# Kernel optimization log

Measured on AMD Instinct MI355X. Metric: run time of the kernel, lower is better.

## Reference

```python
import jax, jax.numpy as jnp
import numpy as np

N_WEIGHTS = 16777216  # 2**24
BATCH = 16777216
PRIOR_SIGMA = 1.0
HALF_LOG_2PI = 0.9189385332046727  # 0.5 * log(2*pi)


def _normal_logprob(x, mu, sigma):
    # Gaussian log density, elementwise
    z = (x - mu) / sigma
    return -0.5 * z * z - jnp.log(sigma) - HALF_LOG_2PI


def setup_inputs() -> dict:
    key = jax.random.key(0)
    k1, k2, k3, k4, k5 = jax.random.split(key, 5)
    noisy_weights = jax.random.normal(k1, (N_WEIGHTS,), dtype=jnp.float32)
    mu_weights = jax.random.normal(k2, (N_WEIGHTS,), dtype=jnp.float32)
    # strictly positive sigmas in [0.5, 1.5)
    sigma_weights = jax.random.uniform(k3, (N_WEIGHTS,), dtype=jnp.float32) + 0.5
    mu_prediction = jax.random.normal(k4, (BATCH,), dtype=jnp.float32)
    sigma_prediction = jnp.float32(0.7)  # single scalar value
    y_true = jax.random.normal(k5, (BATCH,), dtype=jnp.float32)
    return {
        "noisy_weights": noisy_weights,
        "mu_weights": mu_weights,
        "sigma_weights": sigma_weights,
        "mu_prediction": mu_prediction,
        "sigma_prediction": sigma_prediction,
        "y_true": y_true,
    }


def reference(noisy_weights, mu_weights, sigma_weights, mu_prediction, sigma_prediction, y_true):
    # log p(w) under prior N(0, prior_sigma), summed
    loss_prior = _normal_logprob(noisy_weights, 0.0, jnp.float32(PRIOR_SIGMA)).sum()
    # log N(y_true | mu_prediction, sigma_prediction), summed over batch
    loss_likelihood = _normal_logprob(y_true, mu_prediction, sigma_prediction).sum()
    # log q(w | mu_weights, sigma_weights), summed over weights
    loss_variational = _normal_logprob(noisy_weights, mu_weights, sigma_weights).sum()
    # total = variational - prior - likelihood (negative ELBO)
    return loss_variational - loss_prior - loss_likelihood
```

## Files before the change

kernel.cpp:

```cpp
#include <hip/hip_runtime.h>


constexpr int THREADS = 256;
constexpr int ITERS   = 4;
constexpr float LN2          = 0.6931471805599453f;
constexpr float HALF_LOG_2PI = 0.9189385332046727f;

__global__ __launch_bounds__(THREADS, 4) void elbo_partial_fixed(
    const float* __restrict__ xw,
    const float* __restrict__ muw,
    const float* __restrict__ sgw,
    const float* __restrict__ mup,
    const float* __restrict__ sp_ptr,
    const float* __restrict__ yt,
    float* __restrict__ partial)
{
    const float4* x4 = (const float4*)xw;
    const float4* m4 = (const float4*)muw;
    const float4* s4 = (const float4*)sgw;
    const float4* p4 = (const float4*)mup;
    const float4* y4 = (const float4*)yt;

    const int base = blockIdx.x * (THREADS * ITERS) + threadIdx.x;

    float4 xv[ITERS], mv[ITERS], sv[ITERS], pv[ITERS], yv[ITERS];
#pragma unroll
    for (int it = 0; it < ITERS; ++it) {
        int i = base + it * THREADS;
        xv[it] = x4[i];
        mv[it] = m4[i];
        sv[it] = s4[i];
        pv[it] = p4[i];
        yv[it] = y4[i];
    }

    float aw = 0.f;
    float al = 0.f;
    float ab = 0.f;
#pragma unroll
    for (int it = 0; it < ITERS; ++it) {
#define COMP(c) {                                        \
        float dx = xv[it].c - mv[it].c;                  \
        float r  = __builtin_amdgcn_rcpf(sv[it].c);      \
        float z  = dx * r;                               \
        aw += xv[it].c * xv[it].c - z * z;               \
        al += __log2f(sv[it].c);                         \
        float d  = yv[it].c - pv[it].c;                  \
        ab += d * d; }
        COMP(x) COMP(y) COMP(z) COMP(w)
#undef COMP
    }

    float sp = sp_ptr[0];
    float inv2sp2 = 0.5f * __builtin_amdgcn_rcpf(sp * sp);
    float v = 0.5f * aw - LN2 * al + inv2sp2 * ab;

    for (int off = 32; off > 0; off >>= 1)
        v += __shfl_down(v, off);

    __shared__ float lds[THREADS / 64];
    int lane = threadIdx.x & 63;
    int wave = threadIdx.x >> 6;
    if (lane == 0) lds[wave] = v;
    __syncthreads();
    if (threadIdx.x == 0)
        partial[blockIdx.x] = lds[0] + lds[1] + lds[2] + lds[3];
}

__global__ __launch_bounds__(THREADS) void elbo_partial_generic(
    const float* __restrict__ xw,
    const float* __restrict__ muw,
    const float* __restrict__ sgw,
    const float* __restrict__ mup,
    const float* __restrict__ sp_ptr,
    const float* __restrict__ yt,
    float* __restrict__ partial,
    int n4)
{
    const float4* x4 = (const float4*)xw;
    const float4* m4 = (const float4*)muw;
    const float4* s4 = (const float4*)sgw;
    const float4* p4 = (const float4*)mup;
    const float4* y4 = (const float4*)yt;

    float aw = 0.f, al = 0.f, ab = 0.f;
    int idx    = blockIdx.x * blockDim.x + threadIdx.x;
    int stride = gridDim.x * blockDim.x;
    for (int i = idx; i < n4; i += stride) {
        float4 xv = x4[i], mv = m4[i], sv = s4[i], pv = p4[i], yv = y4[i];
#define COMP(c) {                                   \
        float dx = xv.c - mv.c;                     \
        float r  = __builtin_amdgcn_rcpf(sv.c);     \
        float z  = dx * r;                          \
        aw += xv.c * xv.c - z * z;                  \
        al += __log2f(sv.c);                        \
        float d  = yv.c - pv.c;                     \
        ab += d * d; }
        COMP(x) COMP(y) COMP(z) COMP(w)
#undef COMP
    }
    float sp = sp_ptr[0];
    float inv2sp2 = 0.5f * __builtin_amdgcn_rcpf(sp * sp);
    float v = 0.5f * aw - LN2 * al + inv2sp2 * ab;

    for (int off = 32; off > 0; off >>= 1)
        v += __shfl_down(v, off);

    __shared__ float lds[THREADS / 64];
    int lane = threadIdx.x & 63;
    int wave = threadIdx.x >> 6;
    if (lane == 0) lds[wave] = v;
    __syncthreads();
    if (threadIdx.x == 0)
        partial[blockIdx.x] = lds[0] + lds[1] + lds[2] + lds[3];
}

__global__ __launch_bounds__(256) void elbo_final(
    const float* __restrict__ partial,
    const float* __restrict__ sp_ptr,
    float* __restrict__ out,
    int nblocks, float batch_f)
{
    float v = 0.f;
    for (int i = threadIdx.x; i < nblocks; i += 256)
        v += partial[i];
    for (int off = 32; off > 0; off >>= 1)
        v += __shfl_down(v, off);
    __shared__ float lds[4];
    int lane = threadIdx.x & 63;
    int wave = threadIdx.x >> 6;
    if (lane == 0) lds[wave] = v;
    __syncthreads();
    if (threadIdx.x == 0) {
        float sp = sp_ptr[0];
        float c  = batch_f * (logf(sp) + HALF_LOG_2PI);
        out[0] = lds[0] + lds[1] + lds[2] + lds[3] + c;
    }
}

extern "C" void kernel_launch(void* const* d_in, const int* in_sizes, int n_in,
                              void* d_out, int out_size, void* d_ws, size_t ws_size,
                              hipStream_t stream) {
    const float* xw  = (const float*)d_in[0];
    const float* muw = (const float*)d_in[1];
    const float* sgw = (const float*)d_in[2];
    const float* mup = (const float*)d_in[3];
    const float* sp  = (const float*)d_in[4];
    const float* yt  = (const float*)d_in[5];
    float* out     = (float*)d_out;
    float* partial = (float*)d_ws;

    int n  = in_sizes[0];
    int n4 = n / 4;
    const int chunk = THREADS * ITERS;

    int nblocks;
    if (n4 % chunk == 0) {
        nblocks = n4 / chunk;
        elbo_partial_fixed<<<nblocks, THREADS, 0, stream>>>(
            xw, muw, sgw, mup, sp, yt, partial);
    } else {
        nblocks = 2048;
        elbo_partial_generic<<<nblocks, THREADS, 0, stream>>>(
            xw, muw, sgw, mup, sp, yt, partial, n4);
    }
    elbo_final<<<1, 256, 0, stream>>>(partial, sp, out, nblocks,
                                      (float)in_sizes[5]);
}
```

Before: 297.2 us.

## Split weight and prediction terms into separate block ranges of one kernel

```diff
diff --git a/kernel.cpp b/kernel.cpp
--- a/kernel.cpp
+++ b/kernel.cpp
@@ -2,69 +2,95 @@
 
 
 constexpr int THREADS = 256;
-constexpr int ITERS   = 4;
+constexpr int WITERS  = 4;
+constexpr int PITERS  = 8;
 constexpr float LN2          = 0.6931471805599453f;
 constexpr float HALF_LOG_2PI = 0.9189385332046727f;
 
-__global__ __launch_bounds__(THREADS, 4) void elbo_partial_fixed(
+__device__ __forceinline__ float block_reduce(float v, float* lds4) {
+    for (int off = 32; off > 0; off >>= 1)
+        v += __shfl_down(v, off);
+    int lane = threadIdx.x & 63;
+    int wave = threadIdx.x >> 6;
+    if (lane == 0) lds4[wave] = v;
+    __syncthreads();
+    return lds4[0] + lds4[1] + lds4[2] + lds4[3];
+}
+
+__global__ __launch_bounds__(THREADS, 4) void elbo_split(
     const float* __restrict__ xw,
     const float* __restrict__ muw,
     const float* __restrict__ sgw,
     const float* __restrict__ mup,
     const float* __restrict__ sp_ptr,
     const float* __restrict__ yt,
-    float* __restrict__ partial)
+    float* __restrict__ partial,
+    int wblocks)
 {
-    const float4* x4 = (const float4*)xw;
-    const float4* m4 = (const float4*)muw;
-    const float4* s4 = (const float4*)sgw;
-    const float4* p4 = (const float4*)mup;
-    const float4* y4 = (const float4*)yt;
-
-    const int base = blockIdx.x * (THREADS * ITERS) + threadIdx.x;
-
-    float4 xv[ITERS], mv[ITERS], sv[ITERS], pv[ITERS], yv[ITERS];
-#pragma unroll
-    for (int it = 0; it < ITERS; ++it) {
-        int i = base + it * THREADS;
-        xv[it] = x4[i];
-        mv[it] = m4[i];
-        sv[it] = s4[i];
-        pv[it] = p4[i];
-        yv[it] = y4[i];
-    }
-
-    float aw = 0.f;
-    float al = 0.f;
-    float ab = 0.f;
-#pragma unroll
-    for (int it = 0; it < ITERS; ++it) {
-#define COMP(c) {                                        \
-        float dx = xv[it].c - mv[it].c;                  \
-        float r  = __builtin_amdgcn_rcpf(sv[it].c);      \
-        float z  = dx * r;                               \
-        aw += xv[it].c * xv[it].c - z * z;               \
-        al += __log2f(sv[it].c);                         \
-        float d  = yv[it].c - pv[it].c;                  \
-        ab += d * d; }
-        COMP(x) COMP(y) COMP(z) COMP(w)
-#undef COMP
-    }
-
-    float sp = sp_ptr[0];
-    float inv2sp2 = 0.5f * __builtin_amdgcn_rcpf(sp * sp);
-    float v = 0.5f * aw - LN2 * al + inv2sp2 * ab;
-
-    for (int off = 32; off > 0; off >>= 1)
-        v += __shfl_down(v, off);
-
-    __shared__ float lds[THREADS / 64];
-    int lane = threadIdx.x & 63;
-    int wave = threadIdx.x >> 6;
-    if (lane == 0) lds[wave] = v;
-    __syncthreads();
+    __shared__ float lds4[THREADS / 64];
+    const int b = blockIdx.x;
+    float v;
+
+    if (b < wblocks) {
+        const float4* x4 = (const float4*)xw;
+        const float4* m4 = (const float4*)muw;
+        const float4* s4 = (const float4*)sgw;
+        const int base = b * (THREADS * WITERS) + threadIdx.x;
+
+        float4 xv[WITERS], mv[WITERS], sv[WITERS];
+#pragma unroll
+        for (int it = 0; it < WITERS; ++it) {
+            int i = base + it * THREADS;
+            xv[it] = x4[i];
+            mv[it] = m4[i];
+            sv[it] = s4[i];
+        }
+        __builtin_amdgcn_sched_barrier(0);
+
+        float aw = 0.f;
+        float al = 0.f;
+#pragma unroll
+        for (int it = 0; it < WITERS; ++it) {
+#define WCOMP(c) {                                       \
+            float dx = xv[it].c - mv[it].c;              \
+            float r  = __builtin_amdgcn_rcpf(sv[it].c);  \
+            float z  = dx * r;                           \
+            aw += xv[it].c * xv[it].c - z * z;           \
+            al += __log2f(sv[it].c); }
+            WCOMP(x) WCOMP(y) WCOMP(z) WCOMP(w)
+#undef WCOMP
+        }
+        v = 0.5f * aw - LN2 * al;
+    } else {
+        const float4* p4 = (const float4*)mup;
+        const float4* y4 = (const float4*)yt;
+        const int base = (b - wblocks) * (THREADS * PITERS) + threadIdx.x;
+
+        float4 pv[PITERS], yv[PITERS];
+#pragma unroll
+        for (int it = 0; it < PITERS; ++it) {
+            int i = base + it * THREADS;
+            pv[it] = p4[i];
+            yv[it] = y4[i];
+        }
+        __builtin_amdgcn_sched_barrier(0);
+
+        float ab = 0.f;
+#pragma unroll
+        for (int it = 0; it < PITERS; ++it) {
+#define PCOMP(c) {                                       \
+            float d = yv[it].c - pv[it].c;               \
+            ab += d * d; }
+            PCOMP(x) PCOMP(y) PCOMP(z) PCOMP(w)
+#undef PCOMP
+        }
+        float sp = sp_ptr[0];
+        v = 0.5f * __builtin_amdgcn_rcpf(sp * sp) * ab;
+    }
+
+    v = block_reduce(v, lds4);
     if (threadIdx.x == 0)
-        partial[blockIdx.x] = lds[0] + lds[1] + lds[2] + lds[3];
+        partial[b] = v;
 }
 
 __global__ __launch_bounds__(THREADS) void elbo_partial_generic(
@@ -75,7 +101,7 @@
     const float* __restrict__ sp_ptr,
     const float* __restrict__ yt,
     float* __restrict__ partial,
-    int n4)
+    int n4w, int n4p)
 {
     const float4* x4 = (const float4*)xw;
     const float4* m4 = (const float4*)muw;
@@ -86,33 +112,33 @@
     float aw = 0.f, al = 0.f, ab = 0.f;
     int idx    = blockIdx.x * blockDim.x + threadIdx.x;
     int stride = gridDim.x * blockDim.x;
-    for (int i = idx; i < n4; i += stride) {
-        float4 xv = x4[i], mv = m4[i], sv = s4[i], pv = p4[i], yv = y4[i];
-#define COMP(c) {                                   \
+    for (int i = idx; i < n4w; i += stride) {
+        float4 xv = x4[i], mv = m4[i], sv = s4[i];
+#define WCOMP(c) {                                  \
         float dx = xv.c - mv.c;                     \
         float r  = __builtin_amdgcn_rcpf(sv.c);     \
         float z  = dx * r;                          \
         aw += xv.c * xv.c - z * z;                  \
-        al += __log2f(sv.c);                        \
-        float d  = yv.c - pv.c;                     \
+        al += __log2f(sv.c); }
+        WCOMP(x) WCOMP(y) WCOMP(z) WCOMP(w)
+#undef WCOMP
+    }
+    for (int i = idx; i < n4p; i += stride) {
+        float4 pv = p4[i], yv = y4[i];
+#define PCOMP(c) {                                  \
+        float d = yv.c - pv.c;                      \
         ab += d * d; }
-        COMP(x) COMP(y) COMP(z) COMP(w)
-#undef COMP
+        PCOMP(x) PCOMP(y) PCOMP(z) PCOMP(w)
+#undef PCOMP
     }
     float sp = sp_ptr[0];
-    float inv2sp2 = 0.5f * __builtin_amdgcn_rcpf(sp * sp);
-    float v = 0.5f * aw - LN2 * al + inv2sp2 * ab;
-
-    for (int off = 32; off > 0; off >>= 1)
-        v += __shfl_down(v, off);
-
-    __shared__ float lds[THREADS / 64];
-    int lane = threadIdx.x & 63;
-    int wave = threadIdx.x >> 6;
-    if (lane == 0) lds[wave] = v;
-    __syncthreads();
+    float v = 0.5f * aw - LN2 * al
+            + 0.5f * __builtin_amdgcn_rcpf(sp * sp) * ab;
+
+    __shared__ float lds4[THREADS / 64];
+    v = block_reduce(v, lds4);
     if (threadIdx.x == 0)
-        partial[blockIdx.x] = lds[0] + lds[1] + lds[2] + lds[3];
+        partial[blockIdx.x] = v;
 }
 
 __global__ __launch_bounds__(256) void elbo_final(
@@ -150,20 +176,27 @@
     float* out     = (float*)d_out;
     float* partial = (float*)d_ws;
 
-    int n  = in_sizes[0];
-    int n4 = n / 4;
-    const int chunk = THREADS * ITERS;
-
-    int nblocks;
-    if (n4 % chunk == 0) {
-        nblocks = n4 / chunk;
-        elbo_partial_fixed<<<nblocks, THREADS, 0, stream>>>(
-            xw, muw, sgw, mup, sp, yt, partial);
+    int nw  = in_sizes[0];
+    int np  = in_sizes[5];
+    int n4w = nw / 4;
+    int n4p = np / 4;
+    const int wchunk = THREADS * WITERS;
+    const int pchunk = THREADS * PITERS;
+
+    if ((nw % 4 == 0) && (np % 4 == 0) &&
+        (n4w % wchunk == 0) && (n4p % pchunk == 0)) {
+        int wblocks = n4w / wchunk;
+        int pblocks = n4p / pchunk;
+        int nblocks = wblocks + pblocks;
+        elbo_split<<<nblocks, THREADS, 0, stream>>>(
+            xw, muw, sgw, mup, sp, yt, partial, wblocks);
+        elbo_final<<<1, 256, 0, stream>>>(partial, sp, out, nblocks,
+                                          (float)np);
     } else {
-        nblocks = 2048;
+        int nblocks = 2048;
         elbo_partial_generic<<<nblocks, THREADS, 0, stream>>>(
-            xw, muw, sgw, mup, sp, yt, partial, n4);
-    }
-    elbo_final<<<1, 256, 0, stream>>>(partial, sp, out, nblocks,
-                                      (float)in_sizes[5]);
-}
+            xw, muw, sgw, mup, sp, yt, partial, n4w, n4p);
+        elbo_final<<<1, 256, 0, stream>>>(partial, sp, out, nblocks,
+                                          (float)np);
+    }
+}
```

New measurement: 295.3 us. Within noise of the previous version (-0.6%).
